# Kernel tuning notes

Measured on AMD Instinct MI355X. Metric: run time of the kernel, lower is better.

Reference implementation:

```python
import jax, jax.numpy as jnp
import numpy as np

B, S, D, NQ, NS, QN, SN, KC = 128, 128, 100, 50000, 500, 4, 4, 4
RK, HOPS = 10, 3
NEG = -1e9  # masked attention logit (exp -> 0)


def _lin(x, W, b):
    return x @ W.T + b


def _gru(x, h, W_ih, W_hh, b_ih, b_hh):
    # torch.nn.GRUCell math
    gi = _lin(x, W_ih, b_ih)
    gh = _lin(h, W_hh, b_hh)
    i_r, i_z, i_n = jnp.split(gi, 3, axis=-1)
    h_r, h_z, h_n = jnp.split(gh, 3, axis=-1)
    r = jax.nn.sigmoid(i_r + h_r)
    z = jax.nn.sigmoid(i_z + h_z)
    n = jnp.tanh(i_n + r * h_n)
    return (1.0 - z) * n + z * h


def _forward(Eq, Ec, Er, W_ih1, W_hh1, b_ih1, b_hh1, W_ih2, W_hh2, b_ih2, b_hh2,
             Wagg, bagg, W_last, b_last, W_query, b_query, W_key, b_key, W_W, b_W,
             h1_init, h2_init, question, response, mask, q_neighbors, s_neighbors,
             concept_idx, concept_mask):
    Bb, Ss = question.shape
    Dd = Eq.shape[1]
    # detached keys for the rank-k retrieval (matches .clone().detach())
    K_all = jax.lax.stop_gradient(Eq[question])  # [B,S,D]
    pos = jnp.arange(Ss)
    Wq_part, Wk_part = W_W[0, :Dd], W_W[0, Dd:]

    def aggregate(q_t):
        # multi-hop neighbor gather: q->s->q->s, embed alternately, then
        # triangular mean-aggregation sweep with shared per-hop MLPs
        idx = q_t
        levels = [idx]
        for i in range(HOPS):
            idx = (q_neighbors if i % 2 == 0 else s_neighbors)[idx]
            levels.append(idx)
        embs = [(Eq if i % 2 == 0 else Ec)[ix] for i, ix in enumerate(levels)]
        for i in range(HOPS):
            for j in range(HOPS - i):
                embs[j] = jnp.tanh(_lin(embs[j + 1].mean(-2) + embs[j], Wagg[j], bagg[j]))
        return jnp.tanh(_lin(embs[0], W_last, b_last))

    def predict(qc, states, valid):
        # qc [B,KC+1,D], states [B,RK+1,D], valid [RK+1]
        og = jnp.einsum('bqd,bsd->bqs', qc, states)
        Kt = jnp.tanh(_lin(states, W_query, b_query))
        Qt = jnp.tanh(_lin(qc, W_key, b_key))
        tmp = (jnp.einsum('bqd,d->bq', Qt, Wq_part)[:, :, None]
               + jnp.einsum('bsd,d->bs', Kt, Wk_part)[:, None, :] + b_W[0])
        tmp = jnp.where(valid[None, None, :], tmp, NEG)
        alpha = jax.nn.softmax(tmp, axis=2)
        return jnp.sum(alpha * og, axis=(1, 2))

    def step(carry, xs):
        h1, h2, hist, yhat = carry
        t, q_t, r_t, m_t, q_next = xs
        # masked rows use GNN-aggregated question emb, others the raw emb
        emb_q = jnp.where((m_t != 0)[:, None], aggregate(q_t), Eq[q_t])
        h1n = _gru(jnp.concatenate([emb_q, Er[r_t]], axis=1), h1, W_ih1, W_hh1, b_ih1, b_hh1)
        g2 = _gru(h1n, h2, W_ih2, W_hh2, b_ih2, b_hh2)
        # question + zero-padded related-concept embeddings
        emb_qn = Eq[q_next]
        emb_c = Ec[concept_idx[q_next]] * concept_mask[q_next][..., None]
        qc = jnp.concatenate([emb_qn[:, None, :], emb_c], axis=1)
        # rank-k history retrieval on detached embeddings
        scores = jnp.einsum('bsd,bd->bs', K_all, jax.lax.stop_gradient(emb_qn))
        scores = jnp.where(pos[None, :] < t, scores, -jnp.inf)
        _, top_idx = jax.lax.top_k(scores, RK)
        sel = jnp.take_along_axis(hist, top_idx[..., None], axis=1)
        use_topk = t > RK
        hist_states = jnp.where(use_topk, sel, hist[:, :RK])
        states = jnp.concatenate([g2[:, None, :], hist_states], axis=1)
        valid = jnp.concatenate([jnp.ones((1,), bool),
                                 jnp.where(use_topk, True, pos[:RK] < t)])
        p = predict(qc, states, valid)
        # t==0 writes y_hat[:,0]; t>=1 writes y_hat[:,t+1] (column 1 stays 0)
        col = jnp.where(t == 0, 0, t + 1)
        yhat = yhat + p[:, None] * jax.nn.one_hot(col, Ss, dtype=yhat.dtype)
        # original skips h2/history update at t==0 (continue)
        h2n = jnp.where(t == 0, h2, g2)
        histn = jnp.where(t == 0, hist,
                          jax.lax.dynamic_update_slice(hist, g2[:, None, :], (0, t, 0)))
        return (h1n, h2n, histn, yhat), None

    init = (h1_init, h2_init,
            jnp.zeros((Bb, Ss, Dd), jnp.float32), jnp.zeros((Bb, Ss), jnp.float32))
    xs = (jnp.arange(Ss - 1), question[:, :-1].T, response[:, :-1].T,
          mask[:, :-1].T, question[:, 1:].T)
    (_, _, _, yhat), _ = jax.lax.scan(step, init, xs)
    return yhat


def setup_inputs():
    key = jax.random.key(0)
    ks = jax.random.split(key, 32)
    f = lambda i, shape: (jax.random.normal(ks[i], shape) * 0.05).astype(jnp.float32)
    return {
        'Eq': f(0, (NQ, D)), 'Ec': f(1, (NS, D)), 'Er': f(2, (2, D)),
        'W_ih1': f(3, (3 * D, 2 * D)), 'W_hh1': f(4, (3 * D, D)),
        'b_ih1': f(5, (3 * D,)), 'b_hh1': f(6, (3 * D,)),
        'W_ih2': f(7, (3 * D, D)), 'W_hh2': f(8, (3 * D, D)),
        'b_ih2': f(9, (3 * D,)), 'b_hh2': f(10, (3 * D,)),
        'Wagg': f(11, (HOPS, D, D)), 'bagg': f(12, (HOPS, D)),
        'W_last': f(13, (D, D)), 'b_last': f(14, (D,)),
        'W_query': f(15, (D, D)), 'b_query': f(16, (D,)),
        'W_key': f(17, (D, D)), 'b_key': f(18, (D,)),
        'W_W': f(19, (1, 2 * D)), 'b_W': f(20, (1,)),
        'h1_init': f(21, (B, D)), 'h2_init': f(22, (B, D)),
        'question': jax.random.randint(ks[23], (B, S), 0, NQ),
        'response': jax.random.randint(ks[24], (B, S), 0, 2),
        'mask': jax.random.randint(ks[25], (B, S), 0, 2),
        'q_neighbors': jax.random.randint(ks[26], (NQ, QN), 0, NS),
        's_neighbors': jax.random.randint(ks[27], (NS, SN), 0, NQ),
        'concept_idx': jax.random.randint(ks[28], (NQ, KC), 0, NS),
        'concept_mask': jnp.concatenate(
            [jnp.ones((NQ, 1), bool),
             jax.random.randint(ks[29], (NQ, KC - 1), 0, 2).astype(bool)], axis=1),
    }


def reference(Eq, Ec, Er, W_ih1, W_hh1, b_ih1, b_hh1, W_ih2, W_hh2, b_ih2, b_hh2,
              Wagg, bagg, W_last, b_last, W_query, b_query, W_key, b_key, W_W, b_W,
              h1_init, h2_init, question, response, mask, q_neighbors, s_neighbors,
              concept_idx, concept_mask):
    return _forward(Eq, Ec, Er, W_ih1, W_hh1, b_ih1, b_hh1, W_ih2, W_hh2, b_ih2, b_hh2,
                    Wagg, bagg, W_last, b_last, W_query, b_query, W_key, b_key, W_W, b_W,
                    h1_init, h2_init, question, response, mask, q_neighbors, s_neighbors,
                    concept_idx, concept_mask)
```

## Files before the change

### kernel.cpp

```cpp
#include <hip/hip_runtime.h>
#include <hip/hip_bf16.h>
#include <math.h>

typedef unsigned int u32;

#define B_ 128
#define S_ 128
#define T_ 127
#define D_ 100
#define QN_ 4
#define SN_ 4
#define KC_ 4
#define RK_ 10
#define NEGV -1000000000.0f

__device__ __forceinline__ float sigmf(float x) { return 1.0f / (1.0f + expf(-x)); }

__device__ __forceinline__ u32 f2bfbits(float x) {
  __hip_bfloat16 h = __float2bfloat16(x);
  unsigned short s;
  __builtin_memcpy(&s, &h, 2);
  return (u32)s;
}

__global__ __launch_bounds__(256) void setupk(
    const float* Er, const float* W_ih1, const float* b_ih1,
    const float* Wagg, const float* W_last, const float* W_key,
    const float* b_query, const float* W_W, const float* W_query,
    const float* W_hh1, const float* W_hh2, const float* W_ih2,
    const float* b_hh1, const float* b_hh2, const float* b_ih2,
    float* wih1aT, float* erw, float* waggT, float* wlastT, float* wkeyT,
    float* scal, u32* wcat16, float* bcat)
{
  int gid = blockIdx.x * blockDim.x + threadIdx.x;
  int gsz = gridDim.x * blockDim.x;

  for (int x = gid; x < 30000; x += gsz) {
    int j = x / 300, i = x % 300;
    wih1aT[j * 300 + i] = W_ih1[i * 200 + j];
  }
  for (int x = gid; x < 600; x += gsz) {
    int r = x / 300, i = x % 300;
    float acc = b_ih1[i];
    for (int j = 0; j < 100; j++) acc += Er[r * 100 + j] * W_ih1[i * 200 + 100 + j];
    erw[x] = acc;
  }
  for (int x = gid; x < 30000; x += gsz) {
    int h = x / 10000, rr = x % 10000, j = rr / 100, i = rr % 100;
    waggT[h * 10000 + j * 100 + i] = Wagg[h * 10000 + i * 100 + j];
  }
  for (int x = gid; x < 10000; x += gsz) {
    int j = x / 100, i = x % 100;
    wlastT[j * 100 + i] = W_last[i * 100 + j];
    wkeyT[j * 100 + i] = W_key[i * 100 + j];
  }
  for (int x = gid; x < 114688; x += gsz) {
    int slot = x / 64, rem = x % 64, sbu = rem / 16, k = rem % 16;
    const float* src = nullptr;
    if (slot < 300)                       src = W_hh1 + (size_t)slot * 100;
    else if (slot < 600)                  src = W_hh2 + (size_t)(slot - 300) * 100;
    else if (slot >= 1024 && slot < 1324) src = W_ih2 + (size_t)(slot - 1024) * 100;
    else if (slot >= 1536 && slot < 1636) src = W_query + (size_t)(slot - 1536) * 100;
    u32 lo = 0, hi = 0;
    if (src) {
      int e0 = 2 * k, e1 = 2 * k + 1;
      if (e0 < 25) lo = f2bfbits(src[sbu * 25 + e0]);
      if (e1 < 25) hi = f2bfbits(src[sbu * 25 + e1]);
    }
    wcat16[x] = (hi << 16) | lo;
  }
  for (int x = gid; x < 1792; x += gsz) {
    float v = 0.f;
    if (x < 300) v = b_hh1[x];
    else if (x < 600) v = b_hh2[x - 300];
    else if (x >= 1024 && x < 1324) v = b_ih2[x - 1024];
    else if (x >= 1536 && x < 1636) v = b_query[x - 1536];
    bcat[x] = v;
  }
  if (gid == 0) {
    float acc = 0.f;
    for (int i = 0; i < 100; i++) acc += tanhf(b_query[i]) * W_W[100 + i];
    scal[0] = acc;
  }
}

__global__ __launch_bounds__(256) void phaseA(
    const float* Eq, const float* Ec, const int* question, const int* response, const int* mask,
    const int* qnb, const int* snb,
    const float* wih1aT, const float* erw, const float* waggT, const float* wlastT,
    const float* baggf, const float* blastf, float* gi1_all)
{
  const int t = blockIdx.x, b = blockIdx.y, tid = threadIdx.x;
  __shared__ float e0[100], ne0[100], e1[400], ne1[400];
  __shared__ float e2[1600], ne2[1600], m3[1600];
  __shared__ float sum4[400], sum1[100], emq[100];
  __shared__ int l1[4], l2[16], l3[64];

  const int qt = question[b * S_ + t];
  const int mt = mask[b * S_ + t];
  const int rt = response[b * S_ + t];

  if (mt != 0) {
    if (tid < 4) l1[tid] = qnb[qt * QN_ + tid];
    for (int x = tid; x < 100; x += 256) e0[x] = Eq[(size_t)qt * 100 + x];
    __syncthreads();
    if (tid < 16) l2[tid] = snb[l1[tid >> 2] * SN_ + (tid & 3)];
    for (int x = tid; x < 400; x += 256) e1[x] = Ec[(size_t)l1[x / 100] * 100 + (x % 100)];
    __syncthreads();
    if (tid < 64) l3[tid] = qnb[l2[tid >> 2] * QN_ + (tid & 3)];
    for (int x = tid; x < 1600; x += 256) e2[x] = Eq[(size_t)l2[x / 100] * 100 + (x % 100)];
    __syncthreads();
    for (int x = tid; x < 1600; x += 256) {
      int r = x / 100, j = x % 100;
      const int* lr = l3 + r * 4;
      float s = Ec[(size_t)lr[0] * 100 + j] + Ec[(size_t)lr[1] * 100 + j] +
                Ec[(size_t)lr[2] * 100 + j] + Ec[(size_t)lr[3] * 100 + j];
      m3[x] = e2[x] + 0.25f * s;
    }
    for (int x = tid; x < 100; x += 256)
      sum1[x] = e0[x] + 0.25f * (e1[x] + e1[100 + x] + e1[200 + x] + e1[300 + x]);
    for (int x = tid; x < 400; x += 256) {
      int k = x / 100, j = x % 100;
      const float* e2k = e2 + k * 400;
      sum4[x] = e1[x] + 0.25f * (e2k[j] + e2k[100 + j] + e2k[200 + j] + e2k[300 + j]);
    }
    __syncthreads();
    for (int o = tid; o < 2100; o += 256) {
      const float *in, *W;
      float bia;
      float* dst;
      int i = o % 100;
      if (o < 100)      { in = sum1;                           W = waggT;          bia = baggf[i];       dst = ne0 + o; }
      else if (o < 500) { in = sum4 + ((o - 100) / 100) * 100; W = waggT + 10000;  bia = baggf[100 + i]; dst = ne1 + (o - 100); }
      else              { in = m3 + ((o - 500) / 100) * 100;   W = waggT + 20000;  bia = baggf[200 + i]; dst = ne2 + (o - 500); }
      float acc = bia;
      for (int j = 0; j < 100; j++) acc += in[j] * W[j * 100 + i];
      *dst = tanhf(acc);
    }
    __syncthreads();
    for (int x = tid; x < 100; x += 256)
      sum1[x] = ne0[x] + 0.25f * (ne1[x] + ne1[100 + x] + ne1[200 + x] + ne1[300 + x]);
    for (int x = tid; x < 400; x += 256) {
      int k = x / 100, j = x % 100;
      const float* n2k = ne2 + k * 400;
      sum4[x] = ne1[x] + 0.25f * (n2k[j] + n2k[100 + j] + n2k[200 + j] + n2k[300 + j]);
    }
    __syncthreads();
    for (int o = tid; o < 500; o += 256) {
      int i = o % 100;
      if (o < 100) {
        float acc = baggf[i];
        for (int j = 0; j < 100; j++) acc += sum1[j] * waggT[j * 100 + i];
        e0[i] = tanhf(acc);
      } else {
        const float* in = sum4 + ((o - 100) / 100) * 100;
        float acc = baggf[100 + i];
        for (int j = 0; j < 100; j++) acc += in[j] * waggT[10000 + j * 100 + i];
        e1[o - 100] = tanhf(acc);
      }
    }
    __syncthreads();
    for (int x = tid; x < 100; x += 256)
      sum1[x] = e0[x] + 0.25f * (e1[x] + e1[100 + x] + e1[200 + x] + e1[300 + x]);
    __syncthreads();
    for (int o = tid; o < 100; o += 256) {
      float acc = baggf[o];
      for (int j = 0; j < 100; j++) acc += sum1[j] * waggT[j * 100 + o];
      ne0[o] = tanhf(acc);
    }
    __syncthreads();
    for (int o = tid; o < 100; o += 256) {
      float acc = blastf[o];
      for (int j = 0; j < 100; j++) acc += ne0[j] * wlastT[j * 100 + o];
      emq[o] = tanhf(acc);
    }
    __syncthreads();
  } else {
    for (int x = tid; x < 100; x += 256) emq[x] = Eq[(size_t)qt * 100 + x];
    __syncthreads();
  }

  const size_t bt = (size_t)b * T_ + t;
  for (int o = tid; o < 300; o += 256) {
    float acc = erw[rt * 300 + o];
    for (int j = 0; j < 100; j++) acc += emq[j] * wih1aT[j * 300 + o];
    gi1_all[bt * 300 + o] = acc;
  }
}

__global__ __launch_bounds__(128) void phaseB(
    const float* Eq, const float* Ec, const int* question, const int* cidx, const int* cmask,
    const float* wkeyT, const float* b_key, const float* W_W,
    float* qw_all, int* top10_all)
{
  const int t = blockIdx.x, b = blockIdx.y, tid = threadIdx.x;
  const size_t bt = (size_t)b * T_ + t;
  __shared__ float qcf[500];
  __shared__ float qtl[500];
  __shared__ float qwp[20];
  __shared__ float orig[128];
  __shared__ float sval[128];
  __shared__ int sidx[128];
  __shared__ int ci[4], cm[4];

  const int qn = question[b * S_ + t + 1];
  if (tid < 4) { ci[tid] = cidx[qn * KC_ + tid]; cm[tid] = cmask[qn * KC_ + tid]; }
  __syncthreads();

  for (int u = tid; u < 500; u += 128) {
    int row = u / 100, j = u % 100;
    float v;
    if (row == 0) v = Eq[(size_t)qn * 100 + j];
    else {
      int k = row - 1;
      v = cm[k] ? Ec[(size_t)ci[k] * 100 + j] : 0.f;
    }
    qcf[u] = v;
  }
  __syncthreads();
  for (int o = tid; o < 500; o += 128) {
    int q = o / 100, i = o % 100;
    float acc = b_key[i];
    const float* src = qcf + q * 100;
    for (int j = 0; j < 100; j++) acc += src[j] * wkeyT[j * 100 + i];
    qtl[o] = tanhf(acc);
  }
  __syncthreads();
  if (tid < 20) {
    int q = tid / 4, part = tid % 4;
    float acc = 0.f;
    for (int j = part * 25; j < part * 25 + 25; j++) acc += qtl[q * 100 + j] * W_W[j];
    qwp[tid] = acc;
  }
  __syncthreads();
  if (tid < 5) qw_all[bt * 5 + tid] = qwp[tid * 4] + qwp[tid * 4 + 1] + qwp[tid * 4 + 2] + qwp[tid * 4 + 3];

  if (t > RK_) {
    float sc = -__builtin_inff();
    if (tid < t) {
      int qs = question[b * S_ + tid];
      float acc = 0.f;
      for (int j = 0; j < 100; j++) acc += Eq[(size_t)qs * 100 + j] * qcf[j];
      sc = acc;
    }
    orig[tid] = sc;
    __syncthreads();
    for (int pass = 0; pass < 10; pass++) {
      sval[tid] = orig[tid];
      sidx[tid] = tid;
      __syncthreads();
      for (int offt = 64; offt > 0; offt >>= 1) {
        if (tid < offt) {
          float v2 = sval[tid + offt];
          int i2 = sidx[tid + offt];
          if (v2 > sval[tid] || (v2 == sval[tid] && i2 < sidx[tid])) { sval[tid] = v2; sidx[tid] = i2; }
        }
        __syncthreads();
      }
      if (tid == 0) top10_all[bt * 10 + pass] = sidx[0];
      if (tid == sidx[0]) orig[tid] = -__builtin_inff();
      __syncthreads();
    }
  }
}

__device__ __forceinline__ float bf16_dot32(const uint4 w[4], const float hr[32]) {
  float a = 0.f;
#pragma unroll
  for (int c = 0; c < 4; ++c) {
    uint4 ww = w[c];
    const int e = c * 8;
    a = fmaf(__uint_as_float(ww.x << 16),         hr[e + 0], a);
    a = fmaf(__uint_as_float(ww.x & 0xffff0000u), hr[e + 1], a);
    a = fmaf(__uint_as_float(ww.y << 16),         hr[e + 2], a);
    a = fmaf(__uint_as_float(ww.y & 0xffff0000u), hr[e + 3], a);
    a = fmaf(__uint_as_float(ww.z << 16),         hr[e + 4], a);
    a = fmaf(__uint_as_float(ww.z & 0xffff0000u), hr[e + 5], a);
    a = fmaf(__uint_as_float(ww.w << 16),         hr[e + 6], a);
    a = fmaf(__uint_as_float(ww.w & 0xffff0000u), hr[e + 7], a);
  }
  return a;
}

__global__ __launch_bounds__(1024) void seqk(
    const u32* __restrict__ wcat16, const float* __restrict__ bcat,
    const float* __restrict__ gi1_all, const float* __restrict__ qw_all, const int* __restrict__ top10_all,
    const float* __restrict__ W_W, const float* __restrict__ b_W,
    const float* __restrict__ Eq, const float* __restrict__ Ec, const int* __restrict__ question,
    const int* __restrict__ cidx, const int* __restrict__ cmask,
    const float* __restrict__ h1_init, const float* __restrict__ h2_init, const float* __restrict__ scal,
    float* __restrict__ out)
{
  const int b = blockIdx.x, tid = threadIdx.x;
  const int grp = tid >> 2, sub = tid & 3;
  const int ptid = tid - 424;
  const uint4* wimg = (const uint4*)wcat16;

  __shared__ float g2hist[T_ * 100];
  __shared__ float hcomb[200];
  __shared__ __align__(16) float h1n[100], g2v[100];
  __shared__ float gh2[300], kqs[100];
  __shared__ float gi1d[2][300];
  __shared__ float qcd[2][500];
  __shared__ float qwd[2][5];
  __shared__ int topd[2][10];
  __shared__ float kwhist[128];
  __shared__ float ogs[2][55];
  __shared__ float bresS[1792];
  __shared__ float wkS[100];
  __shared__ int cidS[8], cid0S[8];
  __shared__ int qn1S, qnS;
  __shared__ u32 wih2S[300 * 52];
  __shared__ u32 wqS[100 * 52];

  for (int x = tid; x < 1792; x += 1024) bresS[x] = bcat[x];
  if (tid < 100) wkS[tid] = W_W[100 + tid];

  for (int x = tid; x < 300 * 52; x += 1024) {
    int s = x / 52, r = x - s * 52;
    int sb = r / 13, k = r - sb * 13;
    wih2S[x] = wcat16[(size_t)(1024 + s) * 64 + sb * 16 + k];
  }
  for (int x = tid; x < 100 * 52; x += 1024) {
    int s = x / 52, r = x - s * 52;
    int sb = r / 13, k = r - sb * 13;
    wqS[x] = wcat16[(size_t)(1536 + s) * 64 + sb * 16 + k];
  }

  const float bWv = b_W[0];
  const float kw0 = scal[0];

  if (tid < 100) {
    hcomb[tid] = h1_init[b * 100 + tid];
    g2hist[tid] = 0.f;
  } else if (tid < 200) {
    hcomb[tid] = h2_init[b * 100 + (tid - 100)];
  }
  if (tid < 128) kwhist[tid] = kw0;
  if (tid < 300) gi1d[0][tid] = gi1_all[(size_t)b * T_ * 300 + tid];
  if (tid >= 300 && tid < 305) qwd[0][tid - 300] = qw_all[(size_t)b * T_ * 5 + (tid - 300)];
  if (tid == 306) { qn1S = question[b * S_ + 2]; qnS = question[b * S_ + 3]; }
  if (tid >= 320 && tid < 328) {
    int k = tid - 320, qn0 = question[b * S_ + 1];
    cid0S[k] = (k < 4) ? cidx[qn0 * KC_ + k] : cmask[qn0 * KC_ + k - 4];
  }
  if (tid >= 328 && tid < 336) {
    int k = tid - 328, qn1 = question[b * S_ + 2];
    cidS[k] = (k < 4) ? cidx[qn1 * KC_ + k] : cmask[qn1 * KC_ + k - 4];
  }
  __syncthreads();
  if (tid < 500) {
    int q = tid / 100, j = tid % 100;
    int qn0 = question[b * S_ + 1];
    qcd[0][tid] = (q == 0) ? Eq[(size_t)qn0 * 100 + j]
                           : (cid0S[4 + q - 1] ? Ec[(size_t)cid0S[q - 1] * 100 + j] : 0.f);
  }
  __syncthreads();

  for (int t = 0; t < T_; ++t) {
    const size_t bt = (size_t)b * T_ + t;
    const int cur = t & 1, nxt = cur ^ 1;
    const bool pf = (t + 1) < T_;
    const int qn1 = qn1S, qn2 = qnS;

    float pqc = 0.f, pgi = 0.f, pqw = 0.f;
    int ptop = 0, pci = 0, pqn = 0;
    if (pf) {
      if (ptid >= 0 && ptid < 500) {
        int q = ptid / 100, j = ptid % 100;
        pqc = (q == 0) ? Eq[(size_t)qn1 * 100 + j]
                       : (cidS[4 + q - 1] ? Ec[(size_t)cidS[q - 1] * 100 + j] : 0.f);
      }
      if (ptid >= 0 && ptid < 300) pgi = gi1_all[(bt + 1) * 300 + ptid];
      if (tid >= 924 && tid < 929) pqw = qw_all[(bt + 1) * 5 + (tid - 924)];
      if (tid >= 929 && tid < 939 && (t + 1) > RK_) ptop = top10_all[(bt + 1) * 10 + (tid - 929)];
      if (tid >= 939 && tid < 947 && (t + 2) < T_) {
        int k = tid - 939;
        pci = (k < 4) ? cidx[qn2 * KC_ + k] : cmask[qn2 * KC_ + k - 4];
      }
      if (tid == 947) pqn = question[b * S_ + min(t + 4, S_ - 1)];
    }

    if (grp < 200) {
      const bool g1 = (grp < 100);
      const int j = g1 ? grp : (grp - 100);
      const int s0 = g1 ? j : (300 + j);
      uint4 w0[4], w1[4], w2[4];
      {
        const uint4* p0 = wimg + (size_t)s0 * 16 + sub * 4;
        const uint4* p1 = wimg + (size_t)(s0 + 100) * 16 + sub * 4;
        const uint4* p2 = wimg + (size_t)(s0 + 200) * 16 + sub * 4;
#pragma unroll
        for (int c = 0; c < 4; ++c) { w0[c] = p0[c]; w1[c] = p1[c]; w2[c] = p2[c]; }
      }
      float hr[32];
#pragma unroll
      for (int c = 25; c < 32; ++c) hr[c] = 0.f;
      const int off = g1 ? 0 : 100;
#pragma unroll
      for (int c = 0; c < 25; ++c) hr[c] = hcomb[off + sub * 25 + c];
      float a0 = bf16_dot32(w0, hr);
      float a1 = bf16_dot32(w1, hr);
      float a2 = bf16_dot32(w2, hr);
      a0 += __shfl_xor(a0, 1); a0 += __shfl_xor(a0, 2);
      a1 += __shfl_xor(a1, 1); a1 += __shfl_xor(a1, 2);
      a2 += __shfl_xor(a2, 1); a2 += __shfl_xor(a2, 2);
      if (sub == 0) {
        if (g1) {
          float g0 = a0 + bresS[j], gg1 = a1 + bresS[100 + j], gg2 = a2 + bresS[200 + j];
          float rg = sigmf(gi1d[cur][j] + g0);
          float z  = sigmf(gi1d[cur][100 + j] + gg1);
          float n  = tanhf(gi1d[cur][200 + j] + rg * gg2);
          h1n[j] = (1.f - z) * n + z * hcomb[j];
        } else {
          gh2[j]       = a0 + bresS[300 + j];
          gh2[100 + j] = a1 + bresS[400 + j];
          gh2[200 + j] = a2 + bresS[500 + j];
        }
      }
    } else if (grp < 250) {
      int d = grp - 200;
      int s = 1 + d / 5, q = d % 5;
      bool valid = (t > RK_) || (s - 1 < t);
      float a = 0.f;
      if (valid) {
        int idx = (t > RK_) ? topd[cur][s - 1] : (s - 1);
        const float* qcr = &qcd[cur][q * 100 + sub * 25];
        const float* hrow = &g2hist[idx * 100 + sub * 25];
#pragma unroll
        for (int c = 0; c < 25; ++c) a = fmaf(qcr[c], hrow[c], a);
      }
      a += __shfl_xor(a, 1);
      a += __shfl_xor(a, 2);
      if (sub == 0) ogs[cur][s * 5 + q] = a;
    }
    __syncthreads();

    if (grp < 100) {
      const int j = grp;
      const u32* wr0 = wih2S + j * 52 + sub * 13;
      const u32* wr1 = wr0 + 100 * 52;
      const u32* wr2 = wr0 + 200 * 52;
      const float* hsrc = h1n + sub * 25;
      float a0 = 0.f, a1 = 0.f, a2 = 0.f;
#pragma unroll
      for (int k = 0; k < 13; ++k) {
        float h0  = hsrc[2 * k];
        float h1v = (2 * k + 1 < 25) ? hsrc[2 * k + 1] : 0.f;
        u32 w0v = wr0[k], w1v = wr1[k], w2v = wr2[k];
        a0 = fmaf(__uint_as_float(w0v << 16),         h0,  a0);
        a0 = fmaf(__uint_as_float(w0v & 0xffff0000u), h1v, a0);
        a1 = fmaf(__uint_as_float(w1v << 16),         h0,  a1);
        a1 = fmaf(__uint_as_float(w1v & 0xffff0000u), h1v, a1);
        a2 = fmaf(__uint_as_float(w2v << 16),         h0,  a2);
        a2 = fmaf(__uint_as_float(w2v & 0xffff0000u), h1v, a2);
      }
      a0 += __shfl_xor(a0, 1); a0 += __shfl_xor(a0, 2);
      a1 += __shfl_xor(a1, 1); a1 += __shfl_xor(a1, 2);
      a2 += __shfl_xor(a2, 1); a2 += __shfl_xor(a2, 2);
      if (sub == 0) {
        float i_r = a0 + bresS[1024 + j], i_z = a1 + bresS[1124 + j], i_n = a2 + bresS[1224 + j];
        float rg = sigmf(i_r + gh2[j]);
        float z  = sigmf(i_z + gh2[100 + j]);
        float n  = tanhf(i_n + rg * gh2[200 + j]);
        g2v[j] = (1.f - z) * n + z * hcomb[100 + j];
      }
    } else if (tid >= 400 && tid < 500) {
      hcomb[tid - 400] = h1n[tid - 400];
    }
    __syncthreads();

    if (grp < 100) {
      const u32* wq = wqS + grp * 52 + sub * 13;
      const float* hsrc = g2v + sub * 25;
      float a = 0.f;
#pragma unroll
      for (int k = 0; k < 13; ++k) {
        float h0  = hsrc[2 * k];
        float h1v = (2 * k + 1 < 25) ? hsrc[2 * k + 1] : 0.f;
        u32 wv = wq[k];
        a = fmaf(__uint_as_float(wv << 16),         h0,  a);
        a = fmaf(__uint_as_float(wv & 0xffff0000u), h1v, a);
      }
      a += __shfl_xor(a, 1);
      a += __shfl_xor(a, 2);
      if (sub == 0) kqs[grp] = tanhf(a + bresS[1536 + grp]) * wkS[grp];
    } else if (grp < 105) {
      int q = grp - 100;
      const float* qcr = &qcd[cur][q * 100 + sub * 25];
      float a = 0.f;
#pragma unroll
      for (int c = 0; c < 25; ++c) a = fmaf(qcr[c], g2v[sub * 25 + c], a);
      a += __shfl_xor(a, 1);
      a += __shfl_xor(a, 2);
      if (sub == 0) ogs[cur][q] = a;
    }
    if (ptid >= 0) {
      if (pf) {
        if (ptid < 500) qcd[nxt][ptid] = pqc;
        if (ptid < 300) gi1d[nxt][ptid] = pgi;
        if (tid >= 924 && tid < 929) qwd[nxt][tid - 924] = pqw;
        if (tid >= 929 && tid < 939 && (t + 1) > RK_) topd[nxt][tid - 929] = min(T_ - 1, max(0, ptop));
        if (tid >= 939 && tid < 947 && (t + 2) < T_) cidS[tid - 939] = pci;
        if (tid == 947) { qn1S = qn2; qnS = pqn; }
      }
      if (t > 0 && ptid < 100) {
        hcomb[100 + ptid] = g2v[ptid];
        g2hist[t * 100 + ptid] = g2v[ptid];
      }
    }
    __syncthreads();

    if (tid < 64) {
      float v = (tid < 50) ? (kqs[tid] + kqs[tid + 50]) : 0.f;
      v += __shfl_xor(v, 1);
      v += __shfl_xor(v, 2);
      v += __shfl_xor(v, 4);
      v += __shfl_xor(v, 8);
      v += __shfl_xor(v, 16);
      v += __shfl_xor(v, 32);
      const float kw = v;
      float pq = 0.f;
      if (tid < 5) {
        const float qw = qwd[cur][tid];
        float tmp[11];
        float m = -__builtin_inff();
#pragma unroll
        for (int s = 0; s < 11; ++s) {
          float kws;
          bool valid;
          if (s == 0) { kws = kw; valid = true; }
          else if (t > RK_) { kws = kwhist[topd[cur][s - 1]]; valid = true; }
          else { valid = (s - 1 < t); kws = kwhist[s - 1]; }
          float tv = valid ? (qw + kws + bWv) : NEGV;
          tmp[s] = tv;
          m = fmaxf(m, tv);
        }
        float den = 0.f, num = 0.f;
#pragma unroll
        for (int s = 0; s < 11; ++s) {
          float e = expf(tmp[s] - m);
          den += e;
          num += e * ogs[cur][s * 5 + tid];
        }
        pq = num / den;
      }
      if (tid == 5 && t > 0) kwhist[t] = kw;
      float sp = pq;
      sp += __shfl_xor(sp, 1);
      sp += __shfl_xor(sp, 2);
      sp += __shfl_xor(sp, 4);
      if (tid == 0) {
        int col = (t == 0) ? 0 : (t + 1);
        out[b * S_ + col] = sp;
        if (t == 0) out[b * S_ + 1] = 0.f;
      }
    }
  }
}

extern "C" void kernel_launch(void* const* d_in, const int* in_sizes, int n_in,
                              void* d_out, int out_size, void* d_ws, size_t ws_size,
                              hipStream_t stream)
{
  (void)in_sizes; (void)n_in; (void)out_size; (void)ws_size;
  const float* Eq     = (const float*)d_in[0];
  const float* Ec     = (const float*)d_in[1];
  const float* Er     = (const float*)d_in[2];
  const float* W_ih1  = (const float*)d_in[3];
  const float* W_hh1  = (const float*)d_in[4];
  const float* b_ih1  = (const float*)d_in[5];
  const float* b_hh1  = (const float*)d_in[6];
  const float* W_ih2  = (const float*)d_in[7];
  const float* W_hh2  = (const float*)d_in[8];
  const float* b_ih2  = (const float*)d_in[9];
  const float* b_hh2  = (const float*)d_in[10];
  const float* Wagg   = (const float*)d_in[11];
  const float* bagg   = (const float*)d_in[12];
  const float* W_last = (const float*)d_in[13];
  const float* b_last = (const float*)d_in[14];
  const float* W_query= (const float*)d_in[15];
  const float* b_query= (const float*)d_in[16];
  const float* W_key  = (const float*)d_in[17];
  const float* b_key  = (const float*)d_in[18];
  const float* W_W    = (const float*)d_in[19];
  const float* b_W    = (const float*)d_in[20];
  const float* h1_init= (const float*)d_in[21];
  const float* h2_init= (const float*)d_in[22];
  const int* question = (const int*)d_in[23];
  const int* response = (const int*)d_in[24];
  const int* mask     = (const int*)d_in[25];
  const int* qnb      = (const int*)d_in[26];
  const int* snb      = (const int*)d_in[27];
  const int* cidx     = (const int*)d_in[28];
  const int* cmask    = (const int*)d_in[29];
  float* out = (float*)d_out;

  char* ws = (char*)d_ws;
  size_t off = 0;
  auto alloc = [&](size_t bytes) -> void* {
    void* p = ws + off;
    off += (bytes + 255) & ~(size_t)255;
    return p;
  };
  float* wih1aT = (float*)alloc(30000 * 4);
  float* erw    = (float*)alloc(600 * 4);
  float* waggT  = (float*)alloc(30000 * 4);
  float* wlastT = (float*)alloc(10000 * 4);
  float* wkeyT  = (float*)alloc(10000 * 4);
  float* scal   = (float*)alloc(4);
  u32*   wcat16 = (u32*)alloc(114688 * 4);
  float* bcat   = (float*)alloc(1792 * 4);
  float* gi1_all = (float*)alloc((size_t)B_ * T_ * 300 * 4);
  float* qw_all  = (float*)alloc((size_t)B_ * T_ * 5 * 4);
  int*   top10   = (int*)alloc((size_t)B_ * T_ * 10 * 4);

  hipLaunchKernelGGL(setupk, dim3(128), dim3(256), 0, stream,
      Er, W_ih1, b_ih1, Wagg, W_last, W_key, b_query, W_W, W_query,
      W_hh1, W_hh2, W_ih2, b_hh1, b_hh2, b_ih2,
      wih1aT, erw, waggT, wlastT, wkeyT, scal, wcat16, bcat);

  hipLaunchKernelGGL(phaseA, dim3(T_, B_), dim3(256), 0, stream,
      Eq, Ec, question, response, mask, qnb, snb,
      wih1aT, erw, waggT, wlastT, bagg, b_last, gi1_all);

  hipLaunchKernelGGL(phaseB, dim3(T_, B_), dim3(128), 0, stream,
      Eq, Ec, question, cidx, cmask, wkeyT, b_key, W_W,
      qw_all, top10);

  hipLaunchKernelGGL(seqk, dim3(B_), dim3(1024), 0, stream,
      wcat16, bcat, gi1_all, qw_all, top10, W_W, b_W,
      Eq, Ec, question, cidx, cmask,
      h1_init, h2_init, scal, out);
}
```

Measured before the change: 1.499 ms.

## Move GRU1 hidden weights into LDS, spill g2 history to global memory

The per-block g2 history buffer moves from LDS to a global workspace. The freed LDS holds the bf16 W_hh1 weights, so the first GRU's hidden matvec reads from LDS instead of global/L2 each timestep. The og history dot products move to the second phase so they run alongside the W_ih2 matvec. In exchange, history reads go through global memory, relying on cache coherence between a block's own writes and later reads across __syncthreads.

New measurement: 1.397 ms. 1.07x faster.

```diff
diff --git a/kernel.cpp b/kernel.cpp
--- a/kernel.cpp
+++ b/kernel.cpp
@@ -289,14 +289,14 @@
     const float* __restrict__ Eq, const float* __restrict__ Ec, const int* __restrict__ question,
     const int* __restrict__ cidx, const int* __restrict__ cmask,
     const float* __restrict__ h1_init, const float* __restrict__ h2_init, const float* __restrict__ scal,
-    float* __restrict__ out)
+    float* __restrict__ g2hist_g, float* __restrict__ out)
 {
   const int b = blockIdx.x, tid = threadIdx.x;
   const int grp = tid >> 2, sub = tid & 3;
   const int ptid = tid - 424;
   const uint4* wimg = (const uint4*)wcat16;
-
-  __shared__ float g2hist[T_ * 100];
+  float* const g2h = g2hist_g + (size_t)b * (T_ * 128);
+
   __shared__ float hcomb[200];
   __shared__ __align__(16) float h1n[100], g2v[100];
   __shared__ float gh2[300], kqs[100];
@@ -306,19 +306,24 @@
   __shared__ int topd[2][10];
   __shared__ float kwhist[128];
   __shared__ float ogs[2][55];
-  __shared__ float bresS[1792];
+  __shared__ float bresS[1000];
   __shared__ float wkS[100];
   __shared__ int cidS[8], cid0S[8];
   __shared__ int qn1S, qnS;
+  __shared__ u32 whh1S[300 * 52];
   __shared__ u32 wih2S[300 * 52];
   __shared__ u32 wqS[100 * 52];
 
-  for (int x = tid; x < 1792; x += 1024) bresS[x] = bcat[x];
+  for (int x = tid; x < 1000; x += 1024) {
+    int src = (x < 600) ? x : ((x < 900) ? (1024 + (x - 600)) : (1536 + (x - 900)));
+    bresS[x] = bcat[src];
+  }
   if (tid < 100) wkS[tid] = W_W[100 + tid];
 
   for (int x = tid; x < 300 * 52; x += 1024) {
     int s = x / 52, r = x - s * 52;
     int sb = r / 13, k = r - sb * 13;
+    whh1S[x] = wcat16[(size_t)s * 64 + sb * 16 + k];
     wih2S[x] = wcat16[(size_t)(1024 + s) * 64 + sb * 16 + k];
   }
   for (int x = tid; x < 100 * 52; x += 1024) {
@@ -332,10 +337,10 @@
 
   if (tid < 100) {
     hcomb[tid] = h1_init[b * 100 + tid];
-    g2hist[tid] = 0.f;
   } else if (tid < 200) {
     hcomb[tid] = h2_init[b * 100 + (tid - 100)];
   }
+  if (tid >= 200 && tid < 328) g2h[tid - 200] = 0.f;
   if (tid < 128) kwhist[tid] = kw0;
   if (tid < 300) gi1d[0][tid] = gi1_all[(size_t)b * T_ * 300 + tid];
   if (tid >= 300 && tid < 305) qwd[0][tid - 300] = qw_all[(size_t)b * T_ * 5 + (tid - 300)];
@@ -381,67 +386,12 @@
       if (tid == 947) pqn = question[b * S_ + min(t + 4, S_ - 1)];
     }
 
-    if (grp < 200) {
-      const bool g1 = (grp < 100);
-      const int j = g1 ? grp : (grp - 100);
-      const int s0 = g1 ? j : (300 + j);
-      uint4 w0[4], w1[4], w2[4];
-      {
-        const uint4* p0 = wimg + (size_t)s0 * 16 + sub * 4;
-        const uint4* p1 = wimg + (size_t)(s0 + 100) * 16 + sub * 4;
-        const uint4* p2 = wimg + (size_t)(s0 + 200) * 16 + sub * 4;
-#pragma unroll
-        for (int c = 0; c < 4; ++c) { w0[c] = p0[c]; w1[c] = p1[c]; w2[c] = p2[c]; }
-      }
-      float hr[32];
-#pragma unroll
-      for (int c = 25; c < 32; ++c) hr[c] = 0.f;
-      const int off = g1 ? 0 : 100;
-#pragma unroll
-      for (int c = 0; c < 25; ++c) hr[c] = hcomb[off + sub * 25 + c];
-      float a0 = bf16_dot32(w0, hr);
-      float a1 = bf16_dot32(w1, hr);
-      float a2 = bf16_dot32(w2, hr);
-      a0 += __shfl_xor(a0, 1); a0 += __shfl_xor(a0, 2);
-      a1 += __shfl_xor(a1, 1); a1 += __shfl_xor(a1, 2);
-      a2 += __shfl_xor(a2, 1); a2 += __shfl_xor(a2, 2);
-      if (sub == 0) {
-        if (g1) {
-          float g0 = a0 + bresS[j], gg1 = a1 + bresS[100 + j], gg2 = a2 + bresS[200 + j];
-          float rg = sigmf(gi1d[cur][j] + g0);
-          float z  = sigmf(gi1d[cur][100 + j] + gg1);
-          float n  = tanhf(gi1d[cur][200 + j] + rg * gg2);
-          h1n[j] = (1.f - z) * n + z * hcomb[j];
-        } else {
-          gh2[j]       = a0 + bresS[300 + j];
-          gh2[100 + j] = a1 + bresS[400 + j];
-          gh2[200 + j] = a2 + bresS[500 + j];
-        }
-      }
-    } else if (grp < 250) {
-      int d = grp - 200;
-      int s = 1 + d / 5, q = d % 5;
-      bool valid = (t > RK_) || (s - 1 < t);
-      float a = 0.f;
-      if (valid) {
-        int idx = (t > RK_) ? topd[cur][s - 1] : (s - 1);
-        const float* qcr = &qcd[cur][q * 100 + sub * 25];
-        const float* hrow = &g2hist[idx * 100 + sub * 25];
-#pragma unroll
-        for (int c = 0; c < 25; ++c) a = fmaf(qcr[c], hrow[c], a);
-      }
-      a += __shfl_xor(a, 1);
-      a += __shfl_xor(a, 2);
-      if (sub == 0) ogs[cur][s * 5 + q] = a;
-    }
-    __syncthreads();
-
     if (grp < 100) {
       const int j = grp;
-      const u32* wr0 = wih2S + j * 52 + sub * 13;
+      const u32* wr0 = whh1S + j * 52 + sub * 13;
       const u32* wr1 = wr0 + 100 * 52;
       const u32* wr2 = wr0 + 200 * 52;
-      const float* hsrc = h1n + sub * 25;
+      const float* hsrc = hcomb + sub * 25;
       float a0 = 0.f, a1 = 0.f, a2 = 0.f;
 #pragma unroll
       for (int k = 0; k < 13; ++k) {
@@ -459,7 +409,66 @@
       a1 += __shfl_xor(a1, 1); a1 += __shfl_xor(a1, 2);
       a2 += __shfl_xor(a2, 1); a2 += __shfl_xor(a2, 2);
       if (sub == 0) {
-        float i_r = a0 + bresS[1024 + j], i_z = a1 + bresS[1124 + j], i_n = a2 + bresS[1224 + j];
+        float g0 = a0 + bresS[j], gg1 = a1 + bresS[100 + j], gg2 = a2 + bresS[200 + j];
+        float rg = sigmf(gi1d[cur][j] + g0);
+        float z  = sigmf(gi1d[cur][100 + j] + gg1);
+        float n  = tanhf(gi1d[cur][200 + j] + rg * gg2);
+        h1n[j] = (1.f - z) * n + z * hcomb[j];
+      }
+    } else if (grp >= 128 && grp < 228) {
+      const int j = grp - 128;
+      const int s0 = 300 + j;
+      uint4 w0[4], w1[4], w2[4];
+      {
+        const uint4* p0 = wimg + (size_t)s0 * 16 + sub * 4;
+        const uint4* p1 = wimg + (size_t)(s0 + 100) * 16 + sub * 4;
+        const uint4* p2 = wimg + (size_t)(s0 + 200) * 16 + sub * 4;
+#pragma unroll
+        for (int c = 0; c < 4; ++c) { w0[c] = p0[c]; w1[c] = p1[c]; w2[c] = p2[c]; }
+      }
+      float hr[32];
+#pragma unroll
+      for (int c = 25; c < 32; ++c) hr[c] = 0.f;
+#pragma unroll
+      for (int c = 0; c < 25; ++c) hr[c] = hcomb[100 + sub * 25 + c];
+      float a0 = bf16_dot32(w0, hr);
+      float a1 = bf16_dot32(w1, hr);
+      float a2 = bf16_dot32(w2, hr);
+      a0 += __shfl_xor(a0, 1); a0 += __shfl_xor(a0, 2);
+      a1 += __shfl_xor(a1, 1); a1 += __shfl_xor(a1, 2);
+      a2 += __shfl_xor(a2, 1); a2 += __shfl_xor(a2, 2);
+      if (sub == 0) {
+        gh2[j]       = a0 + bresS[300 + j];
+        gh2[100 + j] = a1 + bresS[400 + j];
+        gh2[200 + j] = a2 + bresS[500 + j];
+      }
+    }
+    __syncthreads();
+
+    if (grp < 100) {
+      const int j = grp;
+      const u32* wr0 = wih2S + j * 52 + sub * 13;
+      const u32* wr1 = wr0 + 100 * 52;
+      const u32* wr2 = wr0 + 200 * 52;
+      const float* hsrc = h1n + sub * 25;
+      float a0 = 0.f, a1 = 0.f, a2 = 0.f;
+#pragma unroll
+      for (int k = 0; k < 13; ++k) {
+        float h0  = hsrc[2 * k];
+        float h1v = (2 * k + 1 < 25) ? hsrc[2 * k + 1] : 0.f;
+        u32 w0v = wr0[k], w1v = wr1[k], w2v = wr2[k];
+        a0 = fmaf(__uint_as_float(w0v << 16),         h0,  a0);
+        a0 = fmaf(__uint_as_float(w0v & 0xffff0000u), h1v, a0);
+        a1 = fmaf(__uint_as_float(w1v << 16),         h0,  a1);
+        a1 = fmaf(__uint_as_float(w1v & 0xffff0000u), h1v, a1);
+        a2 = fmaf(__uint_as_float(w2v << 16),         h0,  a2);
+        a2 = fmaf(__uint_as_float(w2v & 0xffff0000u), h1v, a2);
+      }
+      a0 += __shfl_xor(a0, 1); a0 += __shfl_xor(a0, 2);
+      a1 += __shfl_xor(a1, 1); a1 += __shfl_xor(a1, 2);
+      a2 += __shfl_xor(a2, 1); a2 += __shfl_xor(a2, 2);
+      if (sub == 0) {
+        float i_r = a0 + bresS[600 + j], i_z = a1 + bresS[700 + j], i_n = a2 + bresS[800 + j];
         float rg = sigmf(i_r + gh2[j]);
         float z  = sigmf(i_z + gh2[100 + j]);
         float n  = tanhf(i_n + rg * gh2[200 + j]);
@@ -467,6 +476,21 @@
       }
     } else if (tid >= 400 && tid < 500) {
       hcomb[tid - 400] = h1n[tid - 400];
+    } else if (grp >= 128 && grp < 178) {
+      int d = grp - 128;
+      int s = 1 + d / 5, q = d % 5;
+      bool valid = (t > RK_) || (s - 1 < t);
+      float a = 0.f;
+      if (valid) {
+        int idx = (t > RK_) ? topd[cur][s - 1] : (s - 1);
+        const float* qcr = &qcd[cur][q * 100 + sub * 25];
+        const float* hrow = g2h + (size_t)idx * 128 + sub * 25;
+#pragma unroll
+        for (int c = 0; c < 25; ++c) a = fmaf(qcr[c], hrow[c], a);
+      }
+      a += __shfl_xor(a, 1);
+      a += __shfl_xor(a, 2);
+      if (sub == 0) ogs[cur][s * 5 + q] = a;
     }
     __syncthreads();
 
@@ -484,7 +508,7 @@
       }
       a += __shfl_xor(a, 1);
       a += __shfl_xor(a, 2);
-      if (sub == 0) kqs[grp] = tanhf(a + bresS[1536 + grp]) * wkS[grp];
+      if (sub == 0) kqs[grp] = tanhf(a + bresS[900 + grp]) * wkS[grp];
     } else if (grp < 105) {
       int q = grp - 100;
       const float* qcr = &qcd[cur][q * 100 + sub * 25];
@@ -506,7 +530,7 @@
       }
       if (t > 0 && ptid < 100) {
         hcomb[100 + ptid] = g2v[ptid];
-        g2hist[t * 100 + ptid] = g2v[ptid];
+        g2h[(size_t)t * 128 + ptid] = g2v[ptid];
       }
     }
     __syncthreads();
@@ -614,6 +638,7 @@
   float* gi1_all = (float*)alloc((size_t)B_ * T_ * 300 * 4);
   float* qw_all  = (float*)alloc((size_t)B_ * T_ * 5 * 4);
   int*   top10   = (int*)alloc((size_t)B_ * T_ * 10 * 4);
+  float* g2h     = (float*)alloc((size_t)B_ * T_ * 128 * 4);
 
   hipLaunchKernelGGL(setupk, dim3(128), dim3(256), 0, stream,
       Er, W_ih1, b_ih1, Wagg, W_last, W_key, b_query, W_W, W_query,
@@ -631,5 +656,5 @@
   hipLaunchKernelGGL(seqk, dim3(B_), dim3(1024), 0, stream,
       wcat16, bcat, gi1_all, qw_all, top10, W_W, b_W,
       Eq, Ec, question, cidx, cmask,
-      h1_init, h2_init, scal, out);
+      h1_init, h2_init, scal, g2h, out);
 }
```
